# Kernel optimization log

Hardware: AMD Instinct MI355X
Metric: run time of the kernel (lower is better)

## Reference

```python
import jax, jax.numpy as jnp
import numpy as np

P = 2
N_BINS = 15
NUM_CLASSES = 100
N_SRC = 500_000
N_TGT = 500_000


def setup_inputs() -> dict:
    key = jax.random.key(0)
    k1, k2, k3, k4 = jax.random.split(key, 4)
    logits_source = jax.random.normal(k1, (N_SRC, NUM_CLASSES), dtype=jnp.float32)
    labels_source = jax.random.randint(k2, (N_SRC,), 0, NUM_CLASSES, dtype=jnp.int64)
    logits_target = jax.random.normal(k3, (N_TGT, NUM_CLASSES), dtype=jnp.float32)
    weight = jax.random.uniform(k4, (NUM_CLASSES,), dtype=jnp.float32)
    return {"logits_source": logits_source, "labels_source": labels_source,
            "logits_target": logits_target, "weight": weight}


def _equal_mass_edges(conf_target):
    # histedges_equalN: interp(linspace(0, N, n_bins+1), arange(N), sort(conf))
    n = conf_target.shape[0]
    srt = jnp.sort(conf_target)
    xq = jnp.linspace(0.0, float(n), N_BINS + 1)
    xp = jnp.arange(n, dtype=conf_target.dtype)
    return jnp.interp(xq, xp, srt)


def reference(logits_source, labels_source, logits_target, weight):
    sm_s = jax.nn.softmax(logits_source, axis=1)
    sm_t = jax.nn.softmax(logits_target, axis=1)
    conf_s = jnp.max(sm_s, axis=1)              # [Ns]
    pred_s = jnp.argmax(sm_s, axis=1)           # [Ns]
    conf_t = jnp.max(sm_t, axis=1)              # [Nt]
    n_s = conf_s.shape[0]
    n_t = conf_t.shape[0]

    edges = jax.lax.stop_gradient(_equal_mass_edges(conf_t))  # bins from numpy in original
    lo = edges[:-1][:, None]  # [B,1]
    hi = edges[1:][:, None]   # [B,1]

    in_s = (conf_s[None, :] > lo) & (conf_s[None, :] <= hi)   # [B, Ns] bool
    in_t = (conf_t[None, :] > lo) & (conf_t[None, :] <= hi)   # [B, Nt] bool

    acc = (pred_s == labels_source)                           # [Ns] bool
    # per-sample weighted accuracy: weights[label_i] * acc_i
    w_per = weight[labels_source] * acc.astype(weight.dtype)  # [Ns]

    weighted_num = jnp.einsum('bn,n->b', in_s.astype(w_per.dtype), w_per)  # [B]
    count_t = jnp.sum(in_t, axis=1)                                        # [B] int

    normalizer = (n_t - 1) / n_s
    denom = jnp.maximum(count_t - 1, 1).astype(weighted_num.dtype)
    cond_expect = normalizer * weighted_num / denom                        # [B]

    diff_p = jnp.abs(conf_t[None, :] - cond_expect[:, None]) ** P          # [B, Nt]
    per_bin = jnp.sum(in_t.astype(diff_p.dtype) * diff_p, axis=1)          # [B]
    per_bin = jnp.where(count_t > 1, per_bin, 0.0)

    return (jnp.sum(per_bin) / n_t)[None]  # shape [1], matches torch output
```

## Files before the change

kernel.cpp:

```cpp
#include <hip/hip_runtime.h>
#include <math.h>

typedef unsigned int u32;

#define NROWS 500000
#define NCLS  100
#define NBINS 15
#define NRANK 31
#define NSLOT 32
#define TROWS 64
#define HISTB 128

#define OFF_CONF_T 0
#define OFF_CONF_S 2000000
#define OFF_WPER   4000000
#define OFF_CHIST  6000128
#define OFF_SHIST  (OFF_CHIST + 262144)
#define OFF_ACC    (OFF_SHIST + 8388608)
#define OFF_ZEND   (OFF_ACC + 256)
#define OFF_SMAP   OFF_ZEND
#define OFF_META   (OFF_SMAP + 262144)
#define OFF_VALS   (OFF_META + 512)
#define OFF_EDGES  (OFF_VALS + 128)
#define OFF_CE     (OFF_EDGES + 128)

__global__ __launch_bounds__(256) void zero_kernel(u32* __restrict__ p, int n) {
    int i = blockIdx.x * 256 + threadIdx.x;
    if (i < n) p[i] = 0u;
}

__device__ __forceinline__ void merge_ms(float& m, float& s, int& am, float m2, float s2, int am2) {
    if (m2 > m) { s = s * expf(m - m2) + s2; m = m2; am = am2; }
    else        { s += s2 * expf(m2 - m); }
}

__device__ __forceinline__ void row_part(const float* rowp, int qd, float& m, float& s, int& am) {
    m = -__builtin_inff(); am = 0;
    #pragma unroll
    for (int i = 0; i < 25; ++i) {
        float v = rowp[i];
        if (v > m) { m = v; am = qd * 25 + i; }
    }
    s = 0.0f;
    #pragma unroll
    for (int i = 0; i < 25; ++i) s += expf(rowp[i] - m);
}

__global__ __launch_bounds__(256) void conf_kernel(
    const float* __restrict__ logits_t, const float* __restrict__ logits_s,
    const int* __restrict__ labels, const float* __restrict__ weight,
    float* __restrict__ conf_t, float* __restrict__ conf_s,
    float* __restrict__ wper, int tb)
{
    __shared__ float tile[TROWS * NCLS];
    int t = threadIdx.x;
    bool is_src = (int)blockIdx.x >= tb;
    int bid = is_src ? (int)blockIdx.x - tb : (int)blockIdx.x;
    const float* logits = is_src ? logits_s : logits_t;
    int tile0 = bid * TROWS;
    int rows = NROWS - tile0; if (rows > TROWS) rows = TROWS;
    const float4* gp = (const float4*)(logits + (size_t)tile0 * NCLS);
    int nf4 = rows * 25;
    for (int idx = t; idx < nf4; idx += 256) {
        int r = idx / 25, c = idx % 25;
        *(float4*)&tile[r * NCLS + c * 4] = gp[idx];
    }
    __syncthreads();
    int r = t >> 2, qd = t & 3;
    float m, s; int am;
    row_part(&tile[r * NCLS + qd * 25], qd, m, s, am);
    float m2 = __shfl_down(m, 1); float s2 = __shfl_down(s, 1); int am2 = __shfl_down(am, 1);
    merge_ms(m, s, am, m2, s2, am2);
    m2 = __shfl_down(m, 2); s2 = __shfl_down(s, 2); am2 = __shfl_down(am, 2);
    merge_ms(m, s, am, m2, s2, am2);
    if (qd == 0 && r < rows) {
        float c = 1.0f / s;
        if (is_src) {
            conf_s[tile0 + r] = c;
            int lab = labels[tile0 + r];
            wper[tile0 + r] = (am == lab) ? weight[lab] : 0.0f;
        } else {
            conf_t[tile0 + r] = c;
        }
    }
}

__global__ __launch_bounds__(256) void hist_kernel(
    const float* __restrict__ conf, u32* __restrict__ chist)
{
    __shared__ u32 h[1024];
    int t = threadIdx.x;
    for (int i = t; i < 1024; i += 256) h[i] = 0u;
    __syncthreads();
    for (int i = blockIdx.x * 256 + t; i < NROWS; i += HISTB * 256) {
        u32 b = __float_as_uint(conf[i]) >> 16;
        u32 u = b - 15360u;
        if (u < 1024u) atomicAdd(&h[u], 1u);
        else atomicAdd(&chist[b], 1u);
    }
    __syncthreads();
    for (int i = t; i < 1024; i += 256) {
        u32 v = h[i];
        if (v) atomicAdd(&chist[15360 + i], v);
    }
}

__device__ __forceinline__ int rank_of(int q) {
    if (q == NRANK - 1) return NROWS - 1;
    int k = q >> 1;
    int ik = (int)(((long long)k * 100000) / 3);
    return ik + (q & 1);
}

__global__ __launch_bounds__(1024) void rank_prep_kernel(
    const u32* __restrict__ chist, int* __restrict__ smap, int* __restrict__ meta)
{
    __shared__ u32 pre[1024];
    __shared__ u32 wtot[16];
    __shared__ int s_cq[NRANK], s_res[NRANK], s_bin[NRANK];
    __shared__ u32 cd[NRANK * 64];
    __shared__ int s_slotbin[NSLOT];
    __shared__ int s_ns;
    int t = threadIdx.x;
    const uint4* hp = (const uint4*)chist;
    u32 csum = 0;
    for (int j = 0; j < 16; ++j) { uint4 v = hp[t * 16 + j]; csum += v.x + v.y + v.z + v.w; }
    u32 x = csum;
    for (int off = 1; off < 64; off <<= 1) { u32 y = __shfl_up(x, off); if ((t & 63) >= off) x += y; }
    int wv = t >> 6;
    if ((t & 63) == 63) wtot[wv] = x;
    __syncthreads();
    if (t == 0) { u32 run = 0; for (int w = 0; w < 16; ++w) { u32 v = wtot[w]; wtot[w] = run; run += v; } }
    __syncthreads();
    pre[t] = x - csum + wtot[wv];
    __syncthreads();
    if (t < NRANK) {
        u32 r = (u32)rank_of(t);
        int lo = 0, hi = 1023;
        while (lo < hi) { int mid = (lo + hi + 1) >> 1; if (pre[mid] <= r) lo = mid; else hi = mid - 1; }
        s_cq[t] = lo;
        s_res[t] = (int)(r - pre[lo]);
    }
    __syncthreads();
    for (int idx = t; idx < NRANK * 64; idx += 1024) {
        int q = idx >> 6, j = idx & 63;
        cd[idx] = chist[s_cq[q] * 64 + j];
    }
    __syncthreads();
    if (t < NRANK) {
        u32 run = 0; u32 res = (u32)s_res[t]; int bin = 0;
        for (int j = 0; j < 64; ++j) {
            u32 h = cd[t * 64 + j];
            if (res < run + h) { bin = s_cq[t] * 64 + j; s_res[t] = (int)(res - run); break; }
            run += h;
        }
        s_bin[t] = bin;
    }
    __syncthreads();
    if (t == 0) {
        int ns = 0;
        for (int q = 0; q < NRANK; ++q) {
            int b = s_bin[q], sl = -1;
            for (int u = 0; u < ns; ++u) if (s_slotbin[u] == b) { sl = u; break; }
            if (sl < 0) { sl = ns; s_slotbin[ns++] = b; }
            meta[q] = b; meta[32 + q] = s_res[q]; meta[64 + q] = sl;
        }
        s_ns = ns; meta[96] = ns;
        for (int u = ns; u < NSLOT; ++u) s_slotbin[u] = -1;
    }
    __syncthreads();
    int ns = s_ns;
    for (int idx = t; idx < 65536; idx += 1024) {
        int sl = -1;
        for (int u = 0; u < ns; ++u) if (s_slotbin[u] == idx) sl = u;
        smap[idx] = sl;
    }
}

__global__ __launch_bounds__(256) void slot_hist_kernel(
    const float* __restrict__ conf, const int* __restrict__ smap, u32* __restrict__ shist)
{
    int i = blockIdx.x * 256 + threadIdx.x;
    if (i >= NROWS) return;
    u32 b = __float_as_uint(conf[i]);
    int sl = smap[b >> 16];
    if (sl >= 0) atomicAdd(&shist[(size_t)sl * 65536 + (b & 0xFFFFu)], 1u);
}

__global__ __launch_bounds__(1024) void select_kernel(
    const u32* __restrict__ shist, const int* __restrict__ meta, float* __restrict__ vals)
{
    __shared__ u32 wtot[16];
    __shared__ int s_chunk; __shared__ u32 s_base;
    __shared__ u32 cd[64];
    int q = blockIdx.x, t = threadIdx.x;
    int sl = meta[64 + q]; u32 res = (u32)meta[32 + q]; int bin = meta[q];
    const u32* h = shist + (size_t)sl * 65536;
    const uint4* hp = (const uint4*)h;
    u32 csum = 0;
    for (int j = 0; j < 16; ++j) { uint4 v = hp[t * 16 + j]; csum += v.x + v.y + v.z + v.w; }
    u32 x = csum;
    for (int off = 1; off < 64; off <<= 1) { u32 y = __shfl_up(x, off); if ((t & 63) >= off) x += y; }
    int wv = t >> 6;
    if ((t & 63) == 63) wtot[wv] = x;
    __syncthreads();
    if (t == 0) { u32 run = 0; for (int w = 0; w < 16; ++w) { u32 v = wtot[w]; wtot[w] = run; run += v; } }
    __syncthreads();
    u32 prex = x - csum + wtot[wv];
    if (res >= prex && res < prex + csum) { s_chunk = t; s_base = prex; }
    __syncthreads();
    int c = s_chunk;
    if (t < 64) cd[t] = h[c * 64 + t];
    __syncthreads();
    if (t == 0) {
        u32 run = s_base; int low = 0;
        for (int j = 0; j < 64; ++j) {
            u32 hh = cd[j];
            if (res < run + hh) { low = c * 64 + j; break; }
            run += hh;
        }
        vals[q] = __uint_as_float(((u32)bin << 16) | (u32)low);
    }
}

__global__ void edges_kernel(const float* __restrict__ vals, double* __restrict__ edges) {
    if (threadIdx.x == 0 && blockIdx.x == 0) {
        double step = (double)NROWS / 15.0;
        for (int k = 0; k < 16; ++k) {
            double e;
            if (k == 0)       e = (double)vals[0];
            else if (k == 15) e = (double)vals[30];
            else {
                long long ik = ((long long)k * 100000) / 3;
                double frac = (double)k * step - (double)ik;
                double a = (double)vals[2 * k];
                double b = (double)vals[2 * k + 1];
                e = a + frac * (b - a);
            }
            edges[k] = e;
        }
    }
}

__global__ __launch_bounds__(256) void bin_accum_kernel(
    const float* __restrict__ conf_s, const float* __restrict__ wper,
    const float* __restrict__ conf_t, const double* __restrict__ edges,
    float* __restrict__ g_wnum, int* __restrict__ g_cnt)
{
    __shared__ float l_w[NBINS];
    __shared__ int   l_c[NBINS];
    int t = threadIdx.x;
    if (t < NBINS) { l_w[t] = 0.0f; l_c[t] = 0; }
    __syncthreads();
    double e[16];
    #pragma unroll
    for (int j = 0; j < 16; ++j) e[j] = edges[j];
    int i = blockIdx.x * 256 + t;
    if (i < NROWS) {
        double c = (double)conf_s[i];
        int cnt = 0;
        #pragma unroll
        for (int j = 0; j < 16; ++j) cnt += (c > e[j]) ? 1 : 0;
        if (cnt >= 1 && cnt <= NBINS) {
            float w = wper[i];
            if (w != 0.0f) atomicAdd(&l_w[cnt - 1], w);
        }
    } else if (i < 2 * NROWS) {
        double c = (double)conf_t[i - NROWS];
        int cnt = 0;
        #pragma unroll
        for (int j = 0; j < 16; ++j) cnt += (c > e[j]) ? 1 : 0;
        if (cnt >= 1 && cnt <= NBINS) atomicAdd(&l_c[cnt - 1], 1);
    }
    __syncthreads();
    if (t < NBINS) {
        float w = l_w[t];
        int cc = l_c[t];
        if (w != 0.0f) atomicAdd(&g_wnum[t], w);
        if (cc) atomicAdd(&g_cnt[t], cc);
    }
}

__global__ void cond_kernel(const float* __restrict__ g_wnum, const int* __restrict__ g_cnt,
                            double* __restrict__ ce)
{
    int t = threadIdx.x;
    if (t < NBINS) {
        int d = g_cnt[t] - 1; if (d < 1) d = 1;
        ce[t] = ((double)(NROWS - 1) / (double)NROWS) * (double)g_wnum[t] / (double)d;
    }
}

__global__ __launch_bounds__(256) void diff_kernel(
    const float* __restrict__ conf_t, const double* __restrict__ edges,
    const double* __restrict__ ce, float* __restrict__ g_perbin)
{
    __shared__ float l_p[NBINS];
    int t = threadIdx.x;
    if (t < NBINS) l_p[t] = 0.0f;
    __syncthreads();
    double e[16];
    #pragma unroll
    for (int j = 0; j < 16; ++j) e[j] = edges[j];
    int i = blockIdx.x * 256 + t;
    if (i < NROWS) {
        double c = (double)conf_t[i];
        int cnt = 0;
        #pragma unroll
        for (int j = 0; j < 16; ++j) cnt += (c > e[j]) ? 1 : 0;
        if (cnt >= 1 && cnt <= NBINS) {
            double d = c - ce[cnt - 1];
            atomicAdd(&l_p[cnt - 1], (float)(d * d));
        }
    }
    __syncthreads();
    if (t < NBINS) {
        float p = l_p[t];
        if (p != 0.0f) atomicAdd(&g_perbin[t], p);
    }
}

__global__ void final_kernel(const float* __restrict__ g_perbin, const int* __restrict__ g_cnt,
                             float* __restrict__ out)
{
    if (threadIdx.x == 0 && blockIdx.x == 0) {
        double ssum = 0.0;
        for (int b = 0; b < NBINS; ++b)
            if (g_cnt[b] > 1) ssum += (double)g_perbin[b];
        out[0] = (float)(ssum / (double)NROWS);
    }
}

extern "C" void kernel_launch(void* const* d_in, const int* in_sizes, int n_in,
                              void* d_out, int out_size, void* d_ws, size_t ws_size,
                              hipStream_t stream)
{
    const float* logits_s = (const float*)d_in[0];
    const int*   labels   = (const int*)d_in[1];
    const float* logits_t = (const float*)d_in[2];
    const float* weight   = (const float*)d_in[3];

    char* ws = (char*)d_ws;
    float*  conf_t   = (float*)(ws + OFF_CONF_T);
    float*  conf_s   = (float*)(ws + OFF_CONF_S);
    float*  wper     = (float*)(ws + OFF_WPER);
    u32*    chist    = (u32*)(ws + OFF_CHIST);
    u32*    shist    = (u32*)(ws + OFF_SHIST);
    int*    smap     = (int*)(ws + OFF_SMAP);
    int*    meta     = (int*)(ws + OFF_META);
    float*  vals     = (float*)(ws + OFF_VALS);
    double* edges    = (double*)(ws + OFF_EDGES);
    double* ce       = (double*)(ws + OFF_CE);
    float*  g_wnum   = (float*)(ws + OFF_ACC);
    int*    g_cnt    = (int*)(ws + OFF_ACC + 64);
    float*  g_perbin = (float*)(ws + OFF_ACC + 128);
    float*  out      = (float*)d_out;

    int zwords = (OFF_ZEND - OFF_CHIST) / 4;
    zero_kernel<<<(zwords + 255) / 256, 256, 0, stream>>>((u32*)(ws + OFF_CHIST), zwords);

    int tb = (NROWS + TROWS - 1) / TROWS;
    int gb = (NROWS + 255) / 256;
    conf_kernel<<<2 * tb, 256, 0, stream>>>(logits_t, logits_s, labels, weight,
                                            conf_t, conf_s, wper, tb);
    hist_kernel<<<HISTB, 256, 0, stream>>>(conf_t, chist);
    rank_prep_kernel<<<1, 1024, 0, stream>>>(chist, smap, meta);
    slot_hist_kernel<<<gb, 256, 0, stream>>>(conf_t, smap, shist);
    select_kernel<<<NRANK, 1024, 0, stream>>>(shist, meta, vals);
    edges_kernel<<<1, 64, 0, stream>>>(vals, edges);
    bin_accum_kernel<<<(2 * NROWS + 255) / 256, 256, 0, stream>>>(conf_s, wper, conf_t, edges, g_wnum, g_cnt);
    cond_kernel<<<1, 64, 0, stream>>>(g_wnum, g_cnt, ce);
    diff_kernel<<<gb, 256, 0, stream>>>(conf_t, edges, ce, g_perbin);
    final_kernel<<<1, 64, 0, stream>>>(g_perbin, g_cnt, out);
}
```

Before: 568.5 us.

## Use direct global-to-LDS loads, vectorized softmax, sparse slot map, float edges

Loads logit tiles with global_load_lds straight into LDS, contiguous instead of padded per row. Computes row max and exp-sum with float4 registers, xor-shuffle reductions and fast __expf, and picks argmax by comparing the label's logit to the max. Replaces the rank_prep loop that filled a 65536-entry slot map with a zeroed map plus a sparse write of only the used bins, and parallelizes the edges kernel. Converts edges to rounded-down floats so binning compares in fp32 instead of fp64; fast exp and the label-equals-max test can differ from the reference on ties or near bin edges.

```diff
diff --git a/kernel.cpp b/kernel.cpp
--- a/kernel.cpp
+++ b/kernel.cpp
@@ -11,15 +11,17 @@
 #define TROWS 64
 #define HISTB 128
 
+#define NEG_INF (-__builtin_inff())
+
 #define OFF_CONF_T 0
 #define OFF_CONF_S 2000000
 #define OFF_WPER   4000000
 #define OFF_CHIST  6000128
 #define OFF_SHIST  (OFF_CHIST + 262144)
 #define OFF_ACC    (OFF_SHIST + 8388608)
-#define OFF_ZEND   (OFF_ACC + 256)
-#define OFF_SMAP   OFF_ZEND
-#define OFF_META   (OFF_SMAP + 262144)
+#define OFF_SMAP   (OFF_ACC + 256)
+#define OFF_ZEND   (OFF_SMAP + 262144)
+#define OFF_META   OFF_ZEND
 #define OFF_VALS   (OFF_META + 512)
 #define OFF_EDGES  (OFF_VALS + 128)
 #define OFF_CE     (OFF_EDGES + 128)
@@ -27,23 +29,6 @@
 __global__ __launch_bounds__(256) void zero_kernel(u32* __restrict__ p, int n) {
     int i = blockIdx.x * 256 + threadIdx.x;
     if (i < n) p[i] = 0u;
-}
-
-__device__ __forceinline__ void merge_ms(float& m, float& s, int& am, float m2, float s2, int am2) {
-    if (m2 > m) { s = s * expf(m - m2) + s2; m = m2; am = am2; }
-    else        { s += s2 * expf(m2 - m); }
-}
-
-__device__ __forceinline__ void row_part(const float* rowp, int qd, float& m, float& s, int& am) {
-    m = -__builtin_inff(); am = 0;
-    #pragma unroll
-    for (int i = 0; i < 25; ++i) {
-        float v = rowp[i];
-        if (v > m) { m = v; am = qd * 25 + i; }
-    }
-    s = 0.0f;
-    #pragma unroll
-    for (int i = 0; i < 25; ++i) s += expf(rowp[i] - m);
 }
 
 __global__ __launch_bounds__(256) void conf_kernel(
@@ -52,7 +37,7 @@
     float* __restrict__ conf_t, float* __restrict__ conf_s,
     float* __restrict__ wper, int tb)
 {
-    __shared__ float tile[TROWS * NCLS];
+    __shared__ __align__(16) float tile[TROWS * NCLS];
     int t = threadIdx.x;
     bool is_src = (int)blockIdx.x >= tb;
     int bid = is_src ? (int)blockIdx.x - tb : (int)blockIdx.x;
@@ -60,27 +45,66 @@
     int tile0 = bid * TROWS;
     int rows = NROWS - tile0; if (rows > TROWS) rows = TROWS;
     const float4* gp = (const float4*)(logits + (size_t)tile0 * NCLS);
-    int nf4 = rows * 25;
-    for (int idx = t; idx < nf4; idx += 256) {
-        int r = idx / 25, c = idx % 25;
-        *(float4*)&tile[r * NCLS + c * 4] = gp[idx];
-    }
-    __syncthreads();
+    int wv = t >> 6, ln = t & 63;
+
+    if (rows == TROWS) {
+        #pragma unroll
+        for (int k = 0; k < 7; ++k) {
+            int idx = k * 256 + wv * 64 + ln;
+            if (idx < TROWS * 25) {
+                __builtin_amdgcn_global_load_lds(
+                    (const __attribute__((address_space(1))) u32*)(gp + idx),
+                    (__attribute__((address_space(3))) u32*)(&tile[(k * 256 + wv * 64) * 4]),
+                    16, 0, 0);
+            }
+        }
+    } else {
+        int nf4 = rows * 25;
+        for (int idx = t; idx < nf4; idx += 256) {
+            float4 v = gp[idx];
+            *(float4*)&tile[idx * 4] = v;
+        }
+    }
+    __syncthreads();
+
     int r = t >> 2, qd = t & 3;
-    float m, s; int am;
-    row_part(&tile[r * NCLS + qd * 25], qd, m, s, am);
-    float m2 = __shfl_down(m, 1); float s2 = __shfl_down(s, 1); int am2 = __shfl_down(am, 1);
-    merge_ms(m, s, am, m2, s2, am2);
-    m2 = __shfl_down(m, 2); s2 = __shfl_down(s, 2); am2 = __shfl_down(am, 2);
-    merge_ms(m, s, am, m2, s2, am2);
+    const float* rp = &tile[r * NCLS];
+    float4 x[7];
+    #pragma unroll
+    for (int k = 0; k < 6; ++k)
+        x[k] = *(const float4*)(rp + (qd + 4 * k) * 4);
+    x[6] = (qd == 0) ? *(const float4*)(rp + 96)
+                     : make_float4(NEG_INF, NEG_INF, NEG_INF, NEG_INF);
+
+    float4 m4 = x[0];
+    #pragma unroll
+    for (int k = 1; k < 7; ++k) {
+        m4.x = fmaxf(m4.x, x[k].x); m4.y = fmaxf(m4.y, x[k].y);
+        m4.z = fmaxf(m4.z, x[k].z); m4.w = fmaxf(m4.w, x[k].w);
+    }
+    float m = fmaxf(fmaxf(m4.x, m4.y), fmaxf(m4.z, m4.w));
+    m = fmaxf(m, __shfl_xor(m, 1));
+    m = fmaxf(m, __shfl_xor(m, 2));
+
+    float sx = 0.f, sy = 0.f, sz = 0.f, sw = 0.f;
+    #pragma unroll
+    for (int k = 0; k < 7; ++k) {
+        sx += __expf(x[k].x - m); sy += __expf(x[k].y - m);
+        sz += __expf(x[k].z - m); sw += __expf(x[k].w - m);
+    }
+    float s = (sx + sy) + (sz + sw);
+    s += __shfl_xor(s, 1);
+    s += __shfl_xor(s, 2);
+
     if (qd == 0 && r < rows) {
         float c = 1.0f / s;
+        int row = tile0 + r;
         if (is_src) {
-            conf_s[tile0 + r] = c;
-            int lab = labels[tile0 + r];
-            wper[tile0 + r] = (am == lab) ? weight[lab] : 0.0f;
+            conf_s[row] = c;
+            int lab = labels[row];
+            wper[row] = (rp[lab] == m) ? weight[lab] : 0.0f;
         } else {
-            conf_t[tile0 + r] = c;
+            conf_t[row] = c;
         }
     }
 }
@@ -166,15 +190,9 @@
             meta[q] = b; meta[32 + q] = s_res[q]; meta[64 + q] = sl;
         }
         s_ns = ns; meta[96] = ns;
-        for (int u = ns; u < NSLOT; ++u) s_slotbin[u] = -1;
-    }
-    __syncthreads();
-    int ns = s_ns;
-    for (int idx = t; idx < 65536; idx += 1024) {
-        int sl = -1;
-        for (int u = 0; u < ns; ++u) if (s_slotbin[u] == idx) sl = u;
-        smap[idx] = sl;
-    }
+    }
+    __syncthreads();
+    if (t < s_ns) smap[s_slotbin[t]] = t + 1;
 }
 
 __global__ __launch_bounds__(256) void slot_hist_kernel(
@@ -183,7 +201,7 @@
     int i = blockIdx.x * 256 + threadIdx.x;
     if (i >= NROWS) return;
     u32 b = __float_as_uint(conf[i]);
-    int sl = smap[b >> 16];
+    int sl = smap[b >> 16] - 1;
     if (sl >= 0) atomicAdd(&shist[(size_t)sl * 65536 + (b & 0xFFFFu)], 1u);
 }
 
@@ -223,28 +241,31 @@
     }
 }
 
-__global__ void edges_kernel(const float* __restrict__ vals, double* __restrict__ edges) {
-    if (threadIdx.x == 0 && blockIdx.x == 0) {
-        double step = (double)NROWS / 15.0;
-        for (int k = 0; k < 16; ++k) {
-            double e;
-            if (k == 0)       e = (double)vals[0];
-            else if (k == 15) e = (double)vals[30];
-            else {
-                long long ik = ((long long)k * 100000) / 3;
-                double frac = (double)k * step - (double)ik;
-                double a = (double)vals[2 * k];
-                double b = (double)vals[2 * k + 1];
-                e = a + frac * (b - a);
-            }
-            edges[k] = e;
-        }
+__global__ void edges_kernel(const float* __restrict__ vals, double* __restrict__ edges,
+                             float* __restrict__ fedges) {
+    int k = threadIdx.x;
+    if (k < 16) {
+        double e;
+        if (k == 0)       e = (double)vals[0];
+        else if (k == 15) e = (double)vals[30];
+        else {
+            double step = (double)NROWS / 15.0;
+            long long ik = ((long long)k * 100000) / 3;
+            double frac = (double)k * step - (double)ik;
+            double a = (double)vals[2 * k];
+            double b = (double)vals[2 * k + 1];
+            e = a + frac * (b - a);
+        }
+        edges[k] = e;
+        float f = (float)e;
+        if ((double)f > e) f = __uint_as_float(__float_as_uint(f) - 1u);
+        fedges[k] = f;
     }
 }
 
 __global__ __launch_bounds__(256) void bin_accum_kernel(
     const float* __restrict__ conf_s, const float* __restrict__ wper,
-    const float* __restrict__ conf_t, const double* __restrict__ edges,
+    const float* __restrict__ conf_t, const float* __restrict__ fedges,
     float* __restrict__ g_wnum, int* __restrict__ g_cnt)
 {
     __shared__ float l_w[NBINS];
@@ -252,12 +273,12 @@
     int t = threadIdx.x;
     if (t < NBINS) { l_w[t] = 0.0f; l_c[t] = 0; }
     __syncthreads();
-    double e[16];
-    #pragma unroll
-    for (int j = 0; j < 16; ++j) e[j] = edges[j];
+    float e[16];
+    #pragma unroll
+    for (int j = 0; j < 16; ++j) e[j] = fedges[j];
     int i = blockIdx.x * 256 + t;
     if (i < NROWS) {
-        double c = (double)conf_s[i];
+        float c = conf_s[i];
         int cnt = 0;
         #pragma unroll
         for (int j = 0; j < 16; ++j) cnt += (c > e[j]) ? 1 : 0;
@@ -266,7 +287,7 @@
             if (w != 0.0f) atomicAdd(&l_w[cnt - 1], w);
         }
     } else if (i < 2 * NROWS) {
-        double c = (double)conf_t[i - NROWS];
+        float c = conf_t[i - NROWS];
         int cnt = 0;
         #pragma unroll
         for (int j = 0; j < 16; ++j) cnt += (c > e[j]) ? 1 : 0;
@@ -292,24 +313,24 @@
 }
 
 __global__ __launch_bounds__(256) void diff_kernel(
-    const float* __restrict__ conf_t, const double* __restrict__ edges,
+    const float* __restrict__ conf_t, const float* __restrict__ fedges,
     const double* __restrict__ ce, float* __restrict__ g_perbin)
 {
     __shared__ float l_p[NBINS];
     int t = threadIdx.x;
     if (t < NBINS) l_p[t] = 0.0f;
     __syncthreads();
-    double e[16];
-    #pragma unroll
-    for (int j = 0; j < 16; ++j) e[j] = edges[j];
+    float e[16];
+    #pragma unroll
+    for (int j = 0; j < 16; ++j) e[j] = fedges[j];
     int i = blockIdx.x * 256 + t;
     if (i < NROWS) {
-        double c = (double)conf_t[i];
+        float c = conf_t[i];
         int cnt = 0;
         #pragma unroll
         for (int j = 0; j < 16; ++j) cnt += (c > e[j]) ? 1 : 0;
         if (cnt >= 1 && cnt <= NBINS) {
-            double d = c - ce[cnt - 1];
+            double d = (double)c - ce[cnt - 1];
             atomicAdd(&l_p[cnt - 1], (float)(d * d));
         }
     }
@@ -354,6 +375,7 @@
     float*  g_wnum   = (float*)(ws + OFF_ACC);
     int*    g_cnt    = (int*)(ws + OFF_ACC + 64);
     float*  g_perbin = (float*)(ws + OFF_ACC + 128);
+    float*  fedges   = (float*)(ws + OFF_ACC + 192);
     float*  out      = (float*)d_out;
 
     int zwords = (OFF_ZEND - OFF_CHIST) / 4;
@@ -367,9 +389,9 @@
     rank_prep_kernel<<<1, 1024, 0, stream>>>(chist, smap, meta);
     slot_hist_kernel<<<gb, 256, 0, stream>>>(conf_t, smap, shist);
     select_kernel<<<NRANK, 1024, 0, stream>>>(shist, meta, vals);
-    edges_kernel<<<1, 64, 0, stream>>>(vals, edges);
-    bin_accum_kernel<<<(2 * NROWS + 255) / 256, 256, 0, stream>>>(conf_s, wper, conf_t, edges, g_wnum, g_cnt);
+    edges_kernel<<<1, 64, 0, stream>>>(vals, edges, fedges);
+    bin_accum_kernel<<<(2 * NROWS + 255) / 256, 256, 0, stream>>>(conf_s, wper, conf_t, fedges, g_wnum, g_cnt);
     cond_kernel<<<1, 64, 0, stream>>>(g_wnum, g_cnt, ce);
-    diff_kernel<<<gb, 256, 0, stream>>>(conf_t, edges, ce, g_perbin);
+    diff_kernel<<<gb, 256, 0, stream>>>(conf_t, fedges, ce, g_perbin);
     final_kernel<<<1, 64, 0, stream>>>(g_perbin, g_cnt, out);
 }
```

Result: faster. 527.1 us (-7.3%).
